# Performance work log

Hardware: AMD Instinct MI355X
Metric: run time of the kernel (lower is better)

The kernel has to match this reference:

```python
import jax, jax.numpy as jnp
import numpy as np

N = 20000   # nodes
E = 320000  # directed edges (before self-loops)
D = 64      # input_dim
H = 10      # GAT heads
HD = H * D  # 640
NEG_SLOPE = 0.2


def setup_inputs() -> dict:
    key = jax.random.key(0)
    ks = jax.random.split(key, 10)
    return {
        "x": jax.random.normal(ks[0], (N, D), jnp.float32),
        "W_gat": jax.random.normal(ks[1], (D, HD), jnp.float32) / np.sqrt(D).astype(np.float32),
        "att_src": jax.random.normal(ks[2], (H, D), jnp.float32) / np.sqrt(D).astype(np.float32),
        "att_dst": jax.random.normal(ks[3], (H, D), jnp.float32) / np.sqrt(D).astype(np.float32),
        "b_gat": jnp.zeros((HD,), jnp.float32),
        "W_gcn": jax.random.normal(ks[4], (HD, HD), jnp.float32) / np.sqrt(HD).astype(np.float32),
        "b_gcn": jnp.zeros((HD,), jnp.float32),
        "W1": jax.random.normal(ks[5], (2 * HD, 1500), jnp.float32) / np.sqrt(2 * HD).astype(np.float32),
        "b1": jnp.zeros((1500,), jnp.float32),
        "W2": jax.random.normal(ks[6], (1500, 10), jnp.float32) / np.sqrt(1500).astype(np.float32),
        "b2": jnp.zeros((10,), jnp.float32),
        "edge_index": jax.random.randint(ks[7], (2, E), 0, N, dtype=jnp.int64),
    }


def _forward(x, W_gat, att_src, att_dst, b_gat, W_gcn, b_gcn, W1, b1, W2, b2, edge_index):
    n = x.shape[0]
    # add self-loops (PyG default for both GATConv and GCNConv)
    loop = jnp.arange(n, dtype=edge_index.dtype)
    ei = jnp.concatenate([edge_index, jnp.stack([loop, loop])], axis=1)
    src, dst = ei[0], ei[1]

    # ---- GATConv(D -> D, heads=H, concat) ----
    xl = (x @ W_gat).reshape(n, H, D)                      # [N,H,D]
    a_src = jnp.einsum('nhd,hd->nh', xl, att_src)          # [N,H]
    a_dst = jnp.einsum('nhd,hd->nh', xl, att_dst)          # [N,H]
    alpha = jax.nn.leaky_relu(a_src[src] + a_dst[dst], NEG_SLOPE)  # [E',H]
    m = jax.ops.segment_max(alpha, dst, num_segments=n)    # segment softmax over incoming edges
    ex = jnp.exp(alpha - m[dst])
    den = jax.ops.segment_sum(ex, dst, num_segments=n)
    w = ex / (den[dst] + 1e-16)                            # [E',H]
    msg = xl[src] * w[:, :, None]                          # [E',H,D]
    x1 = jax.ops.segment_sum(msg, dst, num_segments=n).reshape(n, HD) + b_gat
    x1 = jax.nn.relu(x1)

    # ---- GCNConv(HD -> HD), symmetric norm with self-loops ----
    deg = jax.ops.segment_sum(jnp.ones(ei.shape[1], x.dtype), dst, num_segments=n)
    dinv = jnp.where(deg > 0, jax.lax.rsqrt(deg), 0.0)
    norm = dinv[src] * dinv[dst]                           # [E']
    xw = x1 @ W_gcn                                        # [N,HD]
    x2 = jax.ops.segment_sum(xw[src] * norm[:, None], dst, num_segments=n) + b_gcn
    x2 = jax.nn.relu(x2)

    # ---- global max/mean pool (batch=None -> single graph) + MLP head ----
    pooled = jnp.concatenate([x2.max(axis=0, keepdims=True),
                              x2.mean(axis=0, keepdims=True)], axis=1)  # [1, 2*HD]
    h = jax.nn.relu(pooled @ W1 + b1)
    # dropout is identity in eval mode
    return h @ W2 + b2                                     # [1, 10]


def reference(x, W_gat, att_src, att_dst, b_gat, W_gcn, b_gcn, W1, b1, W2, b2, edge_index):
    return _forward(x, W_gat, att_src, att_dst, b_gat, W_gcn, b_gcn, W1, b1, W2, b2, edge_index)
```

## Files before the change

### kernel.cpp

```cpp
#include <hip/hip_runtime.h>
#include <hip/hip_bf16.h>
#include <math.h>

#define NN 20000
#define DD 64
#define HH 10
#define HDIM 640
#define NEG 0.2f
#define H1 1500
#define ASTRIDE 12
#define BKK 128

typedef _Float16 half8 __attribute__((ext_vector_type(8)));
typedef _Float16 half4v __attribute__((ext_vector_type(4)));
typedef _Float16 half2v __attribute__((ext_vector_type(2)));
typedef float f32x4 __attribute__((ext_vector_type(4)));

__global__ __launch_bounds__(256) void k_cvtB(const float* __restrict__ Wgcn,
                                              const float* __restrict__ Wg,
                                              _Float16* __restrict__ Wbt,
                                              _Float16* __restrict__ WgT)
{
    __shared__ float t[32][33];
    const int bx = blockIdx.x;
    int by = blockIdx.y;
    const float* W; _Float16* WT; int rows, cols;
    if (by < 20) { W = Wgcn; WT = Wbt; rows = HDIM; cols = HDIM; }
    else         { W = Wg;   WT = WgT; rows = DD;   cols = HDIM; by -= 20; }
    const int lx = threadIdx.x & 31, ly = threadIdx.x >> 5;
    #pragma unroll
    for (int i = ly; i < 32; i += 8)
        t[i][lx] = W[(size_t)(by * 32 + i) * cols + bx * 32 + lx];
    __syncthreads();
    #pragma unroll
    for (int j = ly; j < 32; j += 8)
        WT[(size_t)(bx * 32 + j) * rows + by * 32 + lx] = (_Float16)t[lx][j];
}

__global__ __launch_bounds__(256) void k_gemm1(
    const float* __restrict__ x, const _Float16* __restrict__ WgT,
    const float* __restrict__ att_s, const float* __restrict__ att_d,
    _Float16* __restrict__ xl, float* __restrict__ a_src, float* __restrict__ a_dst)
{
    __shared__ _Float16 As[128][72];
    __shared__ _Float16 Bs[64][72];
    const int tid = threadIdx.x;
    const int m0 = blockIdx.x * 128;
    const int h  = blockIdx.y;
    const int n0 = h * 64;

    {
        const int row = tid >> 1, ch = (tid & 1) * 32;
        const int gr = m0 + row;
        if (gr < NN) {
            const float* xp = &x[(size_t)gr * DD + ch];
            #pragma unroll
            for (int i = 0; i < 8; ++i) {
                const float4 v = *(const float4*)&xp[i * 4];
                half4v o = {(_Float16)v.x, (_Float16)v.y, (_Float16)v.z, (_Float16)v.w};
                *(half4v*)&As[row][ch + i * 4] = o;
            }
        } else {
            const half8 z = {0, 0, 0, 0, 0, 0, 0, 0};
            #pragma unroll
            for (int i = 0; i < 4; ++i) *(half8*)&As[row][ch + i * 8] = z;
        }
    }
    {
        const int row = tid >> 2, part = (tid & 3) * 16;
        const _Float16* wp = &WgT[(size_t)(n0 + row) * DD + part];
        *(half8*)&Bs[row][part]     = *(const half8*)&wp[0];
        *(half8*)&Bs[row][part + 8] = *(const half8*)&wp[8];
    }
    __syncthreads();

    const int lane = tid & 63, wave = tid >> 6;
    const int l15 = lane & 15, quad = lane >> 4;
    f32x4 acc[2][4];
    #pragma unroll
    for (int r = 0; r < 2; ++r)
        #pragma unroll
        for (int c = 0; c < 4; ++c) acc[r][c] = (f32x4){0.f, 0.f, 0.f, 0.f};

    #pragma unroll
    for (int ks = 0; ks < 2; ++ks) {
        const half8 a0 = *(const half8*)&As[wave * 32 + l15][ks * 32 + quad * 8];
        const half8 a1 = *(const half8*)&As[wave * 32 + 16 + l15][ks * 32 + quad * 8];
        #pragma unroll
        for (int c = 0; c < 4; ++c) {
            const half8 b = *(const half8*)&Bs[c * 16 + l15][ks * 32 + quad * 8];
            acc[0][c] = __builtin_amdgcn_mfma_f32_16x16x32_f16(a0, b, acc[0][c], 0, 0, 0);
            acc[1][c] = __builtin_amdgcn_mfma_f32_16x16x32_f16(a1, b, acc[1][c], 0, 0, 0);
        }
    }

    float asv[4], adv[4];
    #pragma unroll
    for (int c = 0; c < 4; ++c) {
        asv[c] = att_s[h * DD + c * 16 + l15];
        adv[c] = att_d[h * DD + c * 16 + l15];
    }
    #pragma unroll
    for (int r = 0; r < 2; ++r) {
        float ps[4] = {0.f, 0.f, 0.f, 0.f}, pd[4] = {0.f, 0.f, 0.f, 0.f};
        #pragma unroll
        for (int c = 0; c < 4; ++c)
            #pragma unroll
            for (int g = 0; g < 4; ++g) {
                ps[g] = fmaf(acc[r][c][g], asv[c], ps[g]);
                pd[g] = fmaf(acc[r][c][g], adv[c], pd[g]);
            }
        #pragma unroll
        for (int m = 1; m <= 8; m <<= 1)
            #pragma unroll
            for (int g = 0; g < 4; ++g) {
                ps[g] += __shfl_xor(ps[g], m);
                pd[g] += __shfl_xor(pd[g], m);
            }
        #pragma unroll
        for (int c = 0; c < 4; ++c)
            #pragma unroll
            for (int g = 0; g < 4; ++g) {
                const int row = m0 + wave * 32 + r * 16 + quad * 4 + g;
                if (row < NN)
                    xl[(size_t)row * HDIM + n0 + c * 16 + l15] = (_Float16)acc[r][c][g];
            }
        if (l15 == 0)
            #pragma unroll
            for (int g = 0; g < 4; ++g) {
                const int row = m0 + wave * 32 + r * 16 + quad * 4 + g;
                if (row < NN) {
                    a_src[(size_t)row * ASTRIDE + h] = ps[g];
                    a_dst[(size_t)row * ASTRIDE + h] = pd[g];
                }
            }
    }
}

__global__ void k_count(const int* __restrict__ ei, int E, int* __restrict__ cnt)
{
    const int e = blockIdx.x * blockDim.x + threadIdx.x;
    if (e >= E + NN) return;
    const int d = (e < E) ? ei[E + e] : (e - E);
    atomicAdd(&cnt[d], 1);
}

__global__ __launch_bounds__(1024) void k_scan(const int* __restrict__ cnt,
                                               int* __restrict__ rowptr,
                                               float* __restrict__ dinv)
{
    __shared__ int sh[1024];
    const int t = threadIdx.x;
    const int CH = 20;
    const int base = t * CH;
    int loc[CH];
    int s = 0;
    #pragma unroll
    for (int i = 0; i < CH; ++i) {
        const int idx = base + i;
        const int c = (idx < NN) ? cnt[idx] : 0;
        loc[i] = s; s += c;
    }
    sh[t] = s; __syncthreads();
    for (int off = 1; off < 1024; off <<= 1) {
        const int v = (t >= off) ? sh[t - off] : 0;
        __syncthreads();
        sh[t] += v;
        __syncthreads();
    }
    const int prev = (t == 0) ? 0 : sh[t - 1];
    #pragma unroll
    for (int i = 0; i < CH; ++i) {
        const int idx = base + i;
        if (idx < NN) {
            rowptr[idx] = prev + loc[i];
            dinv[idx]   = rsqrtf((float)cnt[idx]);
        }
    }
    if (t == 1023) rowptr[NN] = sh[1023];
}

__global__ void k_fill(const int* __restrict__ ei, int E,
                       const int* __restrict__ rowptr,
                       int* __restrict__ cursor, int* __restrict__ csr,
                       const float* __restrict__ dinv, float* __restrict__ wn,
                       const float* __restrict__ aS, const float* __restrict__ aD,
                       float* __restrict__ wgat)
{
    const int e = blockIdx.x * blockDim.x + threadIdx.x;
    if (e >= E + NN) return;
    int s, d;
    if (e < E) { s = ei[e]; d = ei[E + e]; } else { s = d = e - E; }
    const int pos = atomicAdd(&cursor[d], 1);
    const int idx = rowptr[d] + pos;
    csr[idx] = s;
    wn[idx]  = dinv[s] * dinv[d];

    const f32x4 s0 = *(const f32x4*)&aS[(size_t)s * ASTRIDE];
    const f32x4 s1 = *(const f32x4*)&aS[(size_t)s * ASTRIDE + 4];
    const float2 s2 = *(const float2*)&aS[(size_t)s * ASTRIDE + 8];
    const f32x4 d0 = *(const f32x4*)&aD[(size_t)d * ASTRIDE];
    const f32x4 d1 = *(const f32x4*)&aD[(size_t)d * ASTRIDE + 4];
    const float2 d2 = *(const float2*)&aD[(size_t)d * ASTRIDE + 8];
    const float av[10] = {s0.x + d0.x, s0.y + d0.y, s0.z + d0.z, s0.w + d0.w,
                          s1.x + d1.x, s1.y + d1.y, s1.z + d1.z, s1.w + d1.w,
                          s2.x + d2.x, s2.y + d2.y};
    float* wp = &wgat[(size_t)idx * HH];
    #pragma unroll
    for (int h = 0; h < 10; ++h) {
        float a = av[h];
        a = (a >= 0.f) ? a : NEG * a;
        wp[h] = __expf(a);
    }
}

__global__ __launch_bounds__(256) void k_gat_gather(
    const int* __restrict__ rowptr, const int* __restrict__ csr,
    const float* __restrict__ wgat, const _Float16* __restrict__ xl,
    const float* __restrict__ b_gat, _Float16* __restrict__ x1)
{
    const int wave = threadIdx.x >> 6, lane = threadIdx.x & 63;
    const int n = blockIdx.x * 4 + wave;
    const int c0 = lane * 8;
    const int h0 = lane >> 3;
    const bool dual = (lane < 16);
    const int c1 = 512 + lane * 8;
    const int h1 = 8 + (lane >> 3);

    float acc0[8], acc1[8], ws0 = 0.f, ws1 = 0.f;
    #pragma unroll
    for (int i = 0; i < 8; ++i) { acc0[i] = 0.f; acc1[i] = 0.f; }

    const int j0 = rowptr[n], j1 = rowptr[n + 1];
    int j = j0;
    for (; j + 3 < j1; j += 4) {
        const int sA = csr[j], sB = csr[j + 1], sC = csr[j + 2], sD = csr[j + 3];
        const float wA0 = wgat[(size_t)(j + 0) * HH + h0];
        const float wB0 = wgat[(size_t)(j + 1) * HH + h0];
        const float wC0 = wgat[(size_t)(j + 2) * HH + h0];
        const float wD0 = wgat[(size_t)(j + 3) * HH + h0];
        ws0 += wA0 + wB0 + wC0 + wD0;
        const half8 vA0 = *(const half8*)&xl[(size_t)sA * HDIM + c0];
        const half8 vB0 = *(const half8*)&xl[(size_t)sB * HDIM + c0];
        const half8 vC0 = *(const half8*)&xl[(size_t)sC * HDIM + c0];
        const half8 vD0 = *(const half8*)&xl[(size_t)sD * HDIM + c0];
        #pragma unroll
        for (int i = 0; i < 8; ++i) {
            acc0[i] = fmaf(wA0, (float)vA0[i], acc0[i]);
            acc0[i] = fmaf(wB0, (float)vB0[i], acc0[i]);
            acc0[i] = fmaf(wC0, (float)vC0[i], acc0[i]);
            acc0[i] = fmaf(wD0, (float)vD0[i], acc0[i]);
        }
        if (dual) {
            const float wA1 = wgat[(size_t)(j + 0) * HH + h1];
            const float wB1 = wgat[(size_t)(j + 1) * HH + h1];
            const float wC1 = wgat[(size_t)(j + 2) * HH + h1];
            const float wD1 = wgat[(size_t)(j + 3) * HH + h1];
            ws1 += wA1 + wB1 + wC1 + wD1;
            const half8 vA1 = *(const half8*)&xl[(size_t)sA * HDIM + c1];
            const half8 vB1 = *(const half8*)&xl[(size_t)sB * HDIM + c1];
            const half8 vC1 = *(const half8*)&xl[(size_t)sC * HDIM + c1];
            const half8 vD1 = *(const half8*)&xl[(size_t)sD * HDIM + c1];
            #pragma unroll
            for (int i = 0; i < 8; ++i) {
                acc1[i] = fmaf(wA1, (float)vA1[i], acc1[i]);
                acc1[i] = fmaf(wB1, (float)vB1[i], acc1[i]);
                acc1[i] = fmaf(wC1, (float)vC1[i], acc1[i]);
                acc1[i] = fmaf(wD1, (float)vD1[i], acc1[i]);
            }
        }
    }
    for (; j < j1; ++j) {
        const int sA = csr[j];
        const float wA0 = wgat[(size_t)j * HH + h0];
        ws0 += wA0;
        const half8 vA0 = *(const half8*)&xl[(size_t)sA * HDIM + c0];
        #pragma unroll
        for (int i = 0; i < 8; ++i) acc0[i] = fmaf(wA0, (float)vA0[i], acc0[i]);
        if (dual) {
            const float wA1 = wgat[(size_t)j * HH + h1];
            ws1 += wA1;
            const half8 vA1 = *(const half8*)&xl[(size_t)sA * HDIM + c1];
            #pragma unroll
            for (int i = 0; i < 8; ++i) acc1[i] = fmaf(wA1, (float)vA1[i], acc1[i]);
        }
    }

    {
        const float rr = 1.f / (ws0 + 1e-16f);
        const float4 ba = *(const float4*)&b_gat[c0];
        const float4 bb = *(const float4*)&b_gat[c0 + 4];
        const float bv[8] = {ba.x, ba.y, ba.z, ba.w, bb.x, bb.y, bb.z, bb.w};
        half8 o;
        #pragma unroll
        for (int i = 0; i < 8; ++i) {
            const float v = fmaf(acc0[i], rr, bv[i]);
            o[i] = (_Float16)((v > 0.f) ? v : 0.f);
        }
        *(half8*)&x1[(size_t)n * HDIM + c0] = o;
    }
    if (dual) {
        const float rr = 1.f / (ws1 + 1e-16f);
        const float4 ba = *(const float4*)&b_gat[c1];
        const float4 bb = *(const float4*)&b_gat[c1 + 4];
        const float bv[8] = {ba.x, ba.y, ba.z, ba.w, bb.x, bb.y, bb.z, bb.w};
        half8 o;
        #pragma unroll
        for (int i = 0; i < 8; ++i) {
            const float v = fmaf(acc1[i], rr, bv[i]);
            o[i] = (_Float16)((v > 0.f) ? v : 0.f);
        }
        *(half8*)&x1[(size_t)n * HDIM + c1] = o;
    }
}

__global__ __launch_bounds__(256) void k_gcn_gather(
    const int* __restrict__ rowptr, const int* __restrict__ csr,
    const float* __restrict__ wn, const _Float16* __restrict__ x1,
    _Float16* __restrict__ t)
{
    const int wave = threadIdx.x >> 6, lane = threadIdx.x & 63;
    const int n = blockIdx.x * 4 + wave;
    const int c0 = lane * 8;
    const bool dual = (lane < 16);
    const int c1 = 512 + lane * 8;

    float acc0[8], acc1[8];
    #pragma unroll
    for (int i = 0; i < 8; ++i) { acc0[i] = 0.f; acc1[i] = 0.f; }

    const int j0 = rowptr[n], j1 = rowptr[n + 1];
    int j = j0;
    for (; j + 3 < j1; j += 4) {
        const int sA = csr[j], sB = csr[j + 1], sC = csr[j + 2], sD = csr[j + 3];
        const float wA = wn[j], wB = wn[j + 1], wC = wn[j + 2], wD = wn[j + 3];
        const half8 vA0 = *(const half8*)&x1[(size_t)sA * HDIM + c0];
        const half8 vB0 = *(const half8*)&x1[(size_t)sB * HDIM + c0];
        const half8 vC0 = *(const half8*)&x1[(size_t)sC * HDIM + c0];
        const half8 vD0 = *(const half8*)&x1[(size_t)sD * HDIM + c0];
        #pragma unroll
        for (int i = 0; i < 8; ++i) {
            acc0[i] = fmaf(wA, (float)vA0[i], acc0[i]);
            acc0[i] = fmaf(wB, (float)vB0[i], acc0[i]);
            acc0[i] = fmaf(wC, (float)vC0[i], acc0[i]);
            acc0[i] = fmaf(wD, (float)vD0[i], acc0[i]);
        }
        if (dual) {
            const half8 vA1 = *(const half8*)&x1[(size_t)sA * HDIM + c1];
            const half8 vB1 = *(const half8*)&x1[(size_t)sB * HDIM + c1];
            const half8 vC1 = *(const half8*)&x1[(size_t)sC * HDIM + c1];
            const half8 vD1 = *(const half8*)&x1[(size_t)sD * HDIM + c1];
            #pragma unroll
            for (int i = 0; i < 8; ++i) {
                acc1[i] = fmaf(wA, (float)vA1[i], acc1[i]);
                acc1[i] = fmaf(wB, (float)vB1[i], acc1[i]);
                acc1[i] = fmaf(wC, (float)vC1[i], acc1[i]);
                acc1[i] = fmaf(wD, (float)vD1[i], acc1[i]);
            }
        }
    }
    for (; j < j1; ++j) {
        const int sA = csr[j];
        const float wA = wn[j];
        const half8 vA0 = *(const half8*)&x1[(size_t)sA * HDIM + c0];
        #pragma unroll
        for (int i = 0; i < 8; ++i) acc0[i] = fmaf(wA, (float)vA0[i], acc0[i]);
        if (dual) {
            const half8 vA1 = *(const half8*)&x1[(size_t)sA * HDIM + c1];
            #pragma unroll
            for (int i = 0; i < 8; ++i) acc1[i] = fmaf(wA, (float)vA1[i], acc1[i]);
        }
    }

    {
        half8 o;
        #pragma unroll
        for (int i = 0; i < 8; ++i) o[i] = (_Float16)acc0[i];
        *(half8*)&t[(size_t)n * HDIM + c0] = o;
    }
    if (dual) {
        half8 o;
        #pragma unroll
        for (int i = 0; i < 8; ++i) o[i] = (_Float16)acc1[i];
        *(half8*)&t[(size_t)n * HDIM + c1] = o;
    }
}

__global__ __launch_bounds__(256) void k_gemm2(const _Float16* __restrict__ X,
                                               const _Float16* __restrict__ Wbt,
                                               const float* __restrict__ b_gcn,
                                               float* __restrict__ pmax,
                                               float* __restrict__ psum)
{
    __shared__ _Float16 Bs[128 * BKK];
    const int tid = threadIdx.x;
    const int lane = tid & 63, wave = tid >> 6;
    const int l15 = lane & 15, quad = lane >> 4;
    const int m0 = blockIdx.x * 128 + wave * 32;
    const int n0 = blockIdx.y * 128;
    const int l7 = l15 & 7;

    f32x4 acc[2][8];
    #pragma unroll
    for (int r = 0; r < 2; ++r)
        #pragma unroll
        for (int c = 0; c < 8; ++c) acc[r][c] = (f32x4){0.f, 0.f, 0.f, 0.f};

    const int jrow = lane >> 4;
    const int jchunk = lane & 15;

    const _Float16* a0p = &X[(size_t)(m0 + l15) * HDIM + quad * 8];
    const _Float16* a1p = a0p + (size_t)16 * HDIM;

    for (int kb = 0; kb < HDIM; kb += BKK) {
        #pragma unroll
        for (int i = 0; i < 8; ++i) {
            const int r = (wave * 8 + i) * 4 + jrow;
            const int ck = jchunk ^ (r & 7);
            const _Float16* src = &Wbt[(size_t)(n0 + r) * HDIM + kb + ck * 8];
            __builtin_amdgcn_global_load_lds(
                (const __attribute__((address_space(1))) void*)src,
                (__attribute__((address_space(3))) void*)&Bs[(size_t)(wave * 8 + i) * 512],
                16, 0, 0);
        }
        half8 a0[4], a1[4];
        #pragma unroll
        for (int ks = 0; ks < 4; ++ks) {
            a0[ks] = *(const half8*)(a0p + kb + ks * 32);
            a1[ks] = *(const half8*)(a1p + kb + ks * 32);
        }
        __syncthreads();
        #pragma unroll
        for (int ks = 0; ks < 4; ++ks) {
            #pragma unroll
            for (int c = 0; c < 8; ++c) {
                const int br = c * 16 + l15;
                const int ck = (4 * ks + quad) ^ l7;
                const half8 b = *(const half8*)&Bs[(size_t)br * BKK + ck * 8];
                acc[0][c] = __builtin_amdgcn_mfma_f32_16x16x32_f16(a0[ks], b, acc[0][c], 0, 0, 0);
                acc[1][c] = __builtin_amdgcn_mfma_f32_16x16x32_f16(a1[ks], b, acc[1][c], 0, 0, 0);
            }
        }
        __syncthreads();
    }

    float lmax[8], lsum[8];
    #pragma unroll
    for (int c = 0; c < 8; ++c) { lmax[c] = 0.f; lsum[c] = 0.f; }
    #pragma unroll
    for (int c = 0; c < 8; ++c) {
        const float bb = b_gcn[n0 + c * 16 + l15];
        #pragma unroll
        for (int r = 0; r < 2; ++r)
            #pragma unroll
            for (int g = 0; g < 4; ++g) {
                const int row = m0 + r * 16 + quad * 4 + g;
                if (row < NN) {
                    float v = acc[r][c][g] + bb;
                    v = (v > 0.f) ? v : 0.f;
                    lmax[c] = fmaxf(lmax[c], v);
                    lsum[c] += v;
                }
            }
    }
    float* redm = (float*)Bs;
    float* reds = redm + 128;
    if (tid < 128) { redm[tid] = 0.f; reds[tid] = 0.f; }
    __syncthreads();
    #pragma unroll
    for (int c = 0; c < 8; ++c) {
        const int col = c * 16 + l15;
        atomicMax((int*)&redm[col], __float_as_int(lmax[c]));
        atomicAdd(&reds[col], lsum[c]);
    }
    __syncthreads();
    if (tid < 128) {
        atomicMax((int*)&pmax[n0 + tid], __float_as_int(redm[tid]));
        atomicAdd(&psum[n0 + tid], reds[tid]);
    }
}

__global__ __launch_bounds__(256) void k_mlp1(const float* __restrict__ pmax,
                                              const float* __restrict__ psum,
                                              const float* __restrict__ W1,
                                              float* __restrict__ hacc)
{
    __shared__ float pl[80];
    const int t = threadIdx.x;
    const int i0 = blockIdx.y * 80;
    if (t < 80) {
        const int i = i0 + t;
        pl[t] = (i < HDIM) ? pmax[i] : psum[i - HDIM] * (1.0f / NN);
    }
    __syncthreads();
    const int j = blockIdx.x * 256 + t;
    if (j >= H1) return;
    float acc = 0.f;
    #pragma unroll 8
    for (int i = 0; i < 80; ++i)
        acc = fmaf(pl[i], W1[(size_t)(i0 + i) * H1 + j], acc);
    atomicAdd(&hacc[j], acc);
}

__global__ __launch_bounds__(256) void k_mlp2(const float* __restrict__ hacc,
                                              const float* __restrict__ b1,
                                              const float* __restrict__ W2,
                                              const float* __restrict__ b2,
                                              float* __restrict__ out)
{
    __shared__ float hsh[H1];
    __shared__ float red[256];
    const int t = threadIdx.x;
    for (int i = t; i < H1; i += 256) {
        const float v = hacc[i] + b1[i];
        hsh[i] = (v > 0.f) ? v : 0.f;
    }
    __syncthreads();
    float acc[10];
    #pragma unroll
    for (int k = 0; k < 10; ++k) acc[k] = 0.f;
    for (int i = t; i < H1; i += 256) {
        const float h = hsh[i];
        #pragma unroll
        for (int k = 0; k < 10; ++k) acc[k] = fmaf(h, W2[i * 10 + k], acc[k]);
    }
    for (int k = 0; k < 10; ++k) {
        red[t] = acc[k]; __syncthreads();
        for (int s2 = 128; s2 > 0; s2 >>= 1) {
            if (t < s2) red[t] += red[t + s2];
            __syncthreads();
        }
        if (t == 0) out[k] = red[0] + b2[k];
        __syncthreads();
    }
}

extern "C" void kernel_launch(void* const* d_in, const int* in_sizes, int n_in,
                              void* d_out, int out_size, void* d_ws, size_t ws_size,
                              hipStream_t stream)
{
    const float* x     = (const float*)d_in[0];
    const float* Wg    = (const float*)d_in[1];
    const float* att_s = (const float*)d_in[2];
    const float* att_d = (const float*)d_in[3];
    const float* b_gat = (const float*)d_in[4];
    const float* Wgcn  = (const float*)d_in[5];
    const float* b_gcn = (const float*)d_in[6];
    const float* W1    = (const float*)d_in[7];
    const float* b1    = (const float*)d_in[8];
    const float* W2    = (const float*)d_in[9];
    const float* b2    = (const float*)d_in[10];
    const int*   ei    = (const int*)d_in[11];
    const int E = in_sizes[11] / 2;
    const int EP = E + NN;
    float* out = (float*)d_out;

    char* wsp = (char*)d_ws;
    size_t off = 0;
    auto alc = [&](size_t b) { void* p = wsp + off; off += (b + 255) & ~(size_t)255; return p; };
    _Float16* bufA = (_Float16*)alc((size_t)NN * HDIM * 2);
    _Float16* bufB = (_Float16*)alc((size_t)NN * HDIM * 2);
    float* aS     = (float*)alc((size_t)NN * ASTRIDE * 4);
    float* aD     = (float*)alc((size_t)NN * ASTRIDE * 4);
    int*   rowptr = (int*)alc((size_t)(NN + 1) * 4);
    int*   csr    = (int*)alc((size_t)EP * 4);
    float* dinv   = (float*)alc((size_t)NN * 4);
    float* wn     = (float*)alc((size_t)EP * 4);
    float* wgat   = (float*)alc((size_t)EP * HH * 4);
    _Float16* Wbt = (_Float16*)alc((size_t)HDIM * HDIM * 2);
    _Float16* WgT = (_Float16*)alc((size_t)HDIM * DD * 2);
    const size_t zoff = off;
    int*   cnt    = (int*)alc((size_t)NN * 4);
    int*   cursor = (int*)alc((size_t)NN * 4);
    float* pmax   = (float*)alc((size_t)HDIM * 4);
    float* psum   = (float*)alc((size_t)HDIM * 4);
    float* hacc   = (float*)alc((size_t)H1 * 4);
    const size_t zsize = off - zoff;

    hipMemsetAsync(cnt, 0, zsize, stream);

    dim3 gw(HDIM / 32, HDIM / 32 + DD / 32);
    k_cvtB<<<gw, 256, 0, stream>>>(Wgcn, Wg, Wbt, WgT);
    dim3 g1((NN + 127) / 128, HH);
    k_gemm1<<<g1, 256, 0, stream>>>(x, WgT, att_s, att_d, bufA, aS, aD);
    k_count<<<(EP + 255) / 256, 256, 0, stream>>>(ei, E, cnt);
    k_scan<<<1, 1024, 0, stream>>>(cnt, rowptr, dinv);
    k_fill<<<(EP + 255) / 256, 256, 0, stream>>>(ei, E, rowptr, cursor, csr,
                                                 dinv, wn, aS, aD, wgat);
    k_gat_gather<<<NN / 4, 256, 0, stream>>>(rowptr, csr, wgat, bufA, b_gat, bufB);
    k_gcn_gather<<<NN / 4, 256, 0, stream>>>(rowptr, csr, wn, bufB, bufA);
    dim3 g2((NN + 127) / 128, HDIM / 128);
    k_gemm2<<<g2, 256, 0, stream>>>(bufA, Wbt, b_gcn, pmax, psum);
    dim3 gm1(6, 16);
    k_mlp1<<<gm1, 256, 0, stream>>>(pmax, psum, W1, hacc);
    k_mlp2<<<1, 256, 0, stream>>>(hacc, b1, W2, b2, out);
}
```

Before: 367.3 us.

## Split gather edge ranges across two waves and fuse launches via last-block tickets

Both gather kernels now assign two waves to each destination node. Each wave handles half of the node's incoming edge range, and the two partial sums are reduced through shared memory. This doubles parallelism and memory-level concurrency for the latency-bound gathers, at the cost of an extra sync and LDS traffic. Separately, count+scan and mlp1+mlp2 are each fused into one launch using an atomic ticket so the last block finishes the work, which removes two kernel launches.

```diff
diff --git a/kernel.cpp b/kernel.cpp
--- a/kernel.cpp
+++ b/kernel.cpp
@@ -137,18 +137,23 @@
     }
 }
 
-__global__ void k_count(const int* __restrict__ ei, int E, int* __restrict__ cnt)
-{
-    const int e = blockIdx.x * blockDim.x + threadIdx.x;
-    if (e >= E + NN) return;
-    const int d = (e < E) ? ei[E + e] : (e - E);
-    atomicAdd(&cnt[d], 1);
-}
-
-__global__ __launch_bounds__(1024) void k_scan(const int* __restrict__ cnt,
-                                               int* __restrict__ rowptr,
-                                               float* __restrict__ dinv)
-{
+__global__ __launch_bounds__(1024) void k_count_scan(
+    const int* __restrict__ ei, int E, int* __restrict__ cnt,
+    int* __restrict__ rowptr, float* __restrict__ dinv, int* __restrict__ ticket)
+{
+    const int e = blockIdx.x * 1024 + threadIdx.x;
+    if (e < E + NN) {
+        const int d = (e < E) ? ei[E + e] : (e - E);
+        atomicAdd(&cnt[d], 1);
+    }
+    __threadfence();
+    __shared__ int lastf;
+    if (threadIdx.x == 0)
+        lastf = (atomicAdd(ticket, 1) == (int)gridDim.x - 1);
+    __syncthreads();
+    if (!lastf) return;
+    __threadfence();
+
     __shared__ int sh[1024];
     const int t = threadIdx.x;
     const int CH = 20;
@@ -219,8 +224,10 @@
     const float* __restrict__ wgat, const _Float16* __restrict__ xl,
     const float* __restrict__ b_gat, _Float16* __restrict__ x1)
 {
-    const int wave = threadIdx.x >> 6, lane = threadIdx.x & 63;
-    const int n = blockIdx.x * 4 + wave;
+    __shared__ float lsh[2][720];
+    const int wv = threadIdx.x >> 6, lane = threadIdx.x & 63;
+    const int sub = wv >> 1, half = wv & 1;
+    const int n = blockIdx.x * 2 + sub;
     const int c0 = lane * 8;
     const int h0 = lane >> 3;
     const bool dual = (lane < 16);
@@ -231,7 +238,10 @@
     #pragma unroll
     for (int i = 0; i < 8; ++i) { acc0[i] = 0.f; acc1[i] = 0.f; }
 
-    const int j0 = rowptr[n], j1 = rowptr[n + 1];
+    const int r0 = rowptr[n], r1 = rowptr[n + 1];
+    const int mid = (r0 + r1 + 1) >> 1;
+    const int j0 = half ? mid : r0;
+    const int j1 = half ? r1 : mid;
     int j = j0;
     for (; j + 3 < j1; j += 4) {
         const int sA = csr[j], sB = csr[j + 1], sC = csr[j + 2], sD = csr[j + 3];
@@ -286,6 +296,31 @@
         }
     }
 
+    if (half) {
+        float* p = lsh[sub];
+        #pragma unroll
+        for (int i = 0; i < 8; ++i) p[c0 + i] = acc0[i];
+        if (dual) {
+            #pragma unroll
+            for (int i = 0; i < 8; ++i) p[c1 + i] = acc1[i];
+        }
+        p[640 + lane] = ws0;
+        if (dual) p[704 + lane] = ws1;
+    }
+    __syncthreads();
+    if (half) return;
+    {
+        const float* p = lsh[sub];
+        #pragma unroll
+        for (int i = 0; i < 8; ++i) acc0[i] += p[c0 + i];
+        if (dual) {
+            #pragma unroll
+            for (int i = 0; i < 8; ++i) acc1[i] += p[c1 + i];
+        }
+        ws0 += p[640 + lane];
+        if (dual) ws1 += p[704 + lane];
+    }
+
     {
         const float rr = 1.f / (ws0 + 1e-16f);
         const float4 ba = *(const float4*)&b_gat[c0];
@@ -319,8 +354,10 @@
     const float* __restrict__ wn, const _Float16* __restrict__ x1,
     _Float16* __restrict__ t)
 {
-    const int wave = threadIdx.x >> 6, lane = threadIdx.x & 63;
-    const int n = blockIdx.x * 4 + wave;
+    __shared__ float lsh[2][640];
+    const int wv = threadIdx.x >> 6, lane = threadIdx.x & 63;
+    const int sub = wv >> 1, half = wv & 1;
+    const int n = blockIdx.x * 2 + sub;
     const int c0 = lane * 8;
     const bool dual = (lane < 16);
     const int c1 = 512 + lane * 8;
@@ -329,7 +366,10 @@
     #pragma unroll
     for (int i = 0; i < 8; ++i) { acc0[i] = 0.f; acc1[i] = 0.f; }
 
-    const int j0 = rowptr[n], j1 = rowptr[n + 1];
+    const int r0 = rowptr[n], r1 = rowptr[n + 1];
+    const int mid = (r0 + r1 + 1) >> 1;
+    const int j0 = half ? mid : r0;
+    const int j1 = half ? r1 : mid;
     int j = j0;
     for (; j + 3 < j1; j += 4) {
         const int sA = csr[j], sB = csr[j + 1], sC = csr[j + 2], sD = csr[j + 3];
@@ -372,6 +412,27 @@
         }
     }
 
+    if (half) {
+        float* p = lsh[sub];
+        #pragma unroll
+        for (int i = 0; i < 8; ++i) p[c0 + i] = acc0[i];
+        if (dual) {
+            #pragma unroll
+            for (int i = 0; i < 8; ++i) p[c1 + i] = acc1[i];
+        }
+    }
+    __syncthreads();
+    if (half) return;
+    {
+        const float* p = lsh[sub];
+        #pragma unroll
+        for (int i = 0; i < 8; ++i) acc0[i] += p[c0 + i];
+        if (dual) {
+            #pragma unroll
+            for (int i = 0; i < 8; ++i) acc1[i] += p[c1 + i];
+        }
+    }
+
     {
         half8 o;
         #pragma unroll
@@ -480,12 +541,18 @@
     }
 }
 
-__global__ __launch_bounds__(256) void k_mlp1(const float* __restrict__ pmax,
-                                              const float* __restrict__ psum,
-                                              const float* __restrict__ W1,
-                                              float* __restrict__ hacc)
+__global__ __launch_bounds__(256) void k_mlp(const float* __restrict__ pmax,
+                                             const float* __restrict__ psum,
+                                             const float* __restrict__ W1,
+                                             const float* __restrict__ b1,
+                                             const float* __restrict__ W2,
+                                             const float* __restrict__ b2,
+                                             float* __restrict__ hacc,
+                                             int* __restrict__ ticket,
+                                             float* __restrict__ out)
 {
     __shared__ float pl[80];
+    __shared__ int lastf;
     const int t = threadIdx.x;
     const int i0 = blockIdx.y * 80;
     if (t < 80) {
@@ -494,23 +561,22 @@
     }
     __syncthreads();
     const int j = blockIdx.x * 256 + t;
-    if (j >= H1) return;
-    float acc = 0.f;
-    #pragma unroll 8
-    for (int i = 0; i < 80; ++i)
-        acc = fmaf(pl[i], W1[(size_t)(i0 + i) * H1 + j], acc);
-    atomicAdd(&hacc[j], acc);
-}
-
-__global__ __launch_bounds__(256) void k_mlp2(const float* __restrict__ hacc,
-                                              const float* __restrict__ b1,
-                                              const float* __restrict__ W2,
-                                              const float* __restrict__ b2,
-                                              float* __restrict__ out)
-{
+    if (j < H1) {
+        float acc = 0.f;
+        #pragma unroll 8
+        for (int i = 0; i < 80; ++i)
+            acc = fmaf(pl[i], W1[(size_t)(i0 + i) * H1 + j], acc);
+        atomicAdd(&hacc[j], acc);
+    }
+    __threadfence();
+    if (t == 0)
+        lastf = (atomicAdd(ticket, 1) == (int)(gridDim.x * gridDim.y) - 1);
+    __syncthreads();
+    if (!lastf) return;
+    __threadfence();
+
     __shared__ float hsh[H1];
     __shared__ float red[256];
-    const int t = threadIdx.x;
     for (int i = t; i < H1; i += 256) {
         const float v = hacc[i] + b1[i];
         hsh[i] = (v > 0.f) ? v : 0.f;
@@ -575,6 +641,7 @@
     float* pmax   = (float*)alc((size_t)HDIM * 4);
     float* psum   = (float*)alc((size_t)HDIM * 4);
     float* hacc   = (float*)alc((size_t)H1 * 4);
+    int*   tks    = (int*)alc(2 * 4);
     const size_t zsize = off - zoff;
 
     hipMemsetAsync(cnt, 0, zsize, stream);
@@ -583,15 +650,13 @@
     k_cvtB<<<gw, 256, 0, stream>>>(Wgcn, Wg, Wbt, WgT);
     dim3 g1((NN + 127) / 128, HH);
     k_gemm1<<<g1, 256, 0, stream>>>(x, WgT, att_s, att_d, bufA, aS, aD);
-    k_count<<<(EP + 255) / 256, 256, 0, stream>>>(ei, E, cnt);
-    k_scan<<<1, 1024, 0, stream>>>(cnt, rowptr, dinv);
+    k_count_scan<<<(EP + 1023) / 1024, 1024, 0, stream>>>(ei, E, cnt, rowptr, dinv, tks);
     k_fill<<<(EP + 255) / 256, 256, 0, stream>>>(ei, E, rowptr, cursor, csr,
                                                  dinv, wn, aS, aD, wgat);
-    k_gat_gather<<<NN / 4, 256, 0, stream>>>(rowptr, csr, wgat, bufA, b_gat, bufB);
-    k_gcn_gather<<<NN / 4, 256, 0, stream>>>(rowptr, csr, wn, bufB, bufA);
+    k_gat_gather<<<NN / 2, 256, 0, stream>>>(rowptr, csr, wgat, bufA, b_gat, bufB);
+    k_gcn_gather<<<NN / 2, 256, 0, stream>>>(rowptr, csr, wn, bufB, bufA);
     dim3 g2((NN + 127) / 128, HDIM / 128);
     k_gemm2<<<g2, 256, 0, stream>>>(bufA, Wbt, b_gcn, pmax, psum);
     dim3 gm1(6, 16);
-    k_mlp1<<<gm1, 256, 0, stream>>>(pmax, psum, W1, hacc);
-    k_mlp2<<<1, 256, 0, stream>>>(hacc, b1, W2, b2, out);
-}
+    k_mlp<<<gm1, 256, 0, stream>>>(pmax, psum, W1, b1, W2, b2, hacc, tks + 1, out);
+}
```

After: 446.9 us. 1.22x slower.
